# Performance work log

Measured on AMD Instinct MI355X. Metric: run time of the kernel, lower is better.

Reference implementation:

```python
import jax, jax.numpy as jnp
import numpy as np

EPS = 1e-3          # keras BatchNormalization default epsilon
DT = 0.2
LAM2 = 4.0          # lambda_diffusion**2 = 2.0**2
K = 5

def _bn(x, gamma, beta, mean, var):
    # inference-mode batch norm over channel (last) axis
    return (x - mean) * jax.lax.rsqrt(var + EPS) * gamma + beta

def _conv(x, w):
    # NHWC 'same' conv, stride 1, no bias
    return jax.lax.conv_general_dilated(x, w, (1, 1), 'SAME',
                                        dimension_numbers=('NHWC', 'HWIO', 'NHWC'))

def _sobel_edges(x):
    # tf.image.sobel_edges: per-channel 3x3 Sobel with REFLECT padding.
    # returns (dy, dx) matching sobel[...,0], sobel[...,1]
    p = jnp.pad(x, ((0, 0), (1, 1), (1, 1), (0, 0)), mode='reflect')
    dy = (p[:, 2:, :-2] + 2 * p[:, 2:, 1:-1] + p[:, 2:, 2:]) \
       - (p[:, :-2, :-2] + 2 * p[:, :-2, 1:-1] + p[:, :-2, 2:])
    dx = (p[:, :-2, 2:] + 2 * p[:, 1:-1, 2:] + p[:, 2:, 2:]) \
       - (p[:, :-2, :-2] + 2 * p[:, 1:-1, :-2] + p[:, 2:, :-2])
    return dy, dx

def setup_inputs() -> dict:
    key = jax.random.key(0)
    k1, k2, k3 = jax.random.split(key, 3)
    B, H, W, Cin, Cout = 16, 128, 128, 64, 64
    c = jnp.float32
    return {
        'x':   jax.random.normal(k1, (B, H, W, Cin), dtype=c),
        'f_w': jax.random.normal(k2, (3, 3, Cin, Cout), dtype=c) * 0.05,
        'g_w': jax.random.normal(k3, (3, 3, Cout, Cout), dtype=c) * 0.05,
        'bnf_gamma': jnp.ones((Cin,), c),  'bnf_beta': jnp.zeros((Cin,), c),
        'bnf_mean':  jnp.zeros((Cin,), c), 'bnf_var':  jnp.ones((Cin,), c),
        'bng_gamma': jnp.ones((Cout,), c), 'bng_beta': jnp.zeros((Cout,), c),
        'bng_mean':  jnp.zeros((Cout,), c),'bng_var':  jnp.ones((Cout,), c),
        'bno_gamma': jnp.ones((Cout,), c), 'bno_beta': jnp.zeros((Cout,), c),
        'bno_mean':  jnp.zeros((Cout,), c),'bno_var':  jnp.ones((Cout,), c),
    }

def reference(x, f_w, g_w,
              bnf_gamma, bnf_beta, bnf_mean, bnf_var,
              bng_gamma, bng_beta, bng_mean, bng_var,
              bno_gamma, bno_beta, bno_mean, bno_var):
    f = _conv(jax.nn.relu(_bn(x, bnf_gamma, bnf_beta, bnf_mean, bnf_var)), f_w)
    h = f
    g = _conv(jax.nn.relu(_bn(h, bng_gamma, bng_beta, bng_mean, bng_var)), g_w)
    g1 = g
    dy, dx = _sobel_edges(h)
    Dx = 1.0 / (dy * dy / LAM2 + 1.0)   # source: sobel[..., 0]
    Dy = 1.0 / (dx * dx / LAM2 + 1.0)   # source: sobel[..., 1]
    # NOTE: faithful to source — rolls on axis=2 (W) and axis=3 (channels in NHWC)
    ux = 0.5 * (jnp.roll(g, 1, axis=2) - jnp.roll(g, -1, axis=2))
    vy = 0.5 * (jnp.roll(g1, 1, axis=3) - jnp.roll(g1, -1, axis=3))
    Ax = g * DT
    Ay = g1 * DT
    Bx = Dx * DT
    By = Dy * DT
    E = (ux + vy) * DT
    D = 1.0 / (1.0 + 2 * Bx + 2 * By)
    h0 = h
    for _ in range(K):
        prev = h
        h = D * ((1 - 2 * Bx - 2 * By) * h0
                 - 2 * E * h
                 + (-Ax + 2 * Bx) * jnp.roll(h, 1, axis=2)
                 + ( Ax + 2 * Bx) * jnp.roll(h, -1, axis=2)
                 + (-Ay + 2 * By) * jnp.roll(h, 1, axis=3)
                 + ( Ay + 2 * By) * jnp.roll(h, -1, axis=3)
                 + 2 * DT * f)
        h0 = prev
    h = jax.nn.relu(_bn(h, bno_gamma, bno_beta, bno_mean, bno_var))
    return (h, g)
```

## Files before the change

### kernel.cpp

```cpp
#include <hip/hip_runtime.h>

#define HH 128
#define WW 128
#define CC 64
#define ROW (WW*CC)
#define SLOTB 128
#define ROWB (130*SLOTB)
#define FSTR 68

typedef _Float16 half8 __attribute__((ext_vector_type(8)));
typedef _Float16 half4v __attribute__((ext_vector_type(4)));
typedef float floatx4 __attribute__((ext_vector_type(4)));

__device__ inline floatx4 rcp4(floatx4 v)
{
    floatx4 r;
    r[0] = __builtin_amdgcn_rcpf(v[0]);
    r[1] = __builtin_amdgcn_rcpf(v[1]);
    r[2] = __builtin_amdgcn_rcpf(v[2]);
    r[3] = __builtin_amdgcn_rcpf(v[3]);
    return r;
}

__global__ __launch_bounds__(256)
void repack_w(const float* __restrict__ wf, const float* __restrict__ wg,
              _Float16* __restrict__ W2f, _Float16* __restrict__ W2g)
{
    int idx = blockIdx.x * 256 + threadIdx.x;
    int sel = idx >= 36864;
    int id  = sel ? idx - 36864 : idx;
    const float* src = sel ? wg : wf;
    _Float16* dst = sel ? W2g : W2f;
    int t = id >> 12, c = (id >> 6) & 63, o = id & 63;
    int kc = c >> 5, q = (c >> 3) & 3, j = c & 7;
    int pos = ((((t*2 + kc)*4 + q)*64 + o) << 3) + j;
    dst[pos] = (_Float16)src[id];
}

template<int BNIN, int EPI>
__global__ __launch_bounds__(512, 2)
void conv_mfma(const void* __restrict__ srcv, const _Float16* __restrict__ W2,
               _Float16* __restrict__ outH, float* __restrict__ outF,
               _Float16* __restrict__ y2,
               const float* __restrict__ ig, const float* __restrict__ ib,
               const float* __restrict__ imu, const float* __restrict__ iva,
               const float* __restrict__ og, const float* __restrict__ ob,
               const float* __restrict__ om, const float* __restrict__ ov)
{
    __shared__ __align__(16) char smem[69632];
    const int t = threadIdx.x;
    const int blk = ((blockIdx.x & 7) << 7) | (blockIdx.x >> 3);
    const int b = blk >> 6, i0 = (blk & 63) * 2;

    const int c8 = (t & 7) << 3;
    float scv[8], biv[8];
    if (BNIN) {
        #pragma unroll
        for (int j = 0; j < 8; ++j) {
            float s = ig[c8+j] * rsqrtf(iva[c8+j] + 1e-3f);
            scv[j] = s; biv[j] = ib[c8+j] - imu[c8+j]*s;
        }
    }

    if (t < 256) {
        int rr = t >> 6, s = (t >> 5) & 1;
        *(float*)(smem + rr*ROWB + (s ? 129*SLOTB : 0) + ((t & 31) << 2)) = 0.f;
    }

    if (BNIN) {
        for (int r = 0; r < 4; ++r) {
            int iy = i0 - 1 + r;
            bool inb = (iy >= 0) && (iy < HH);
            #pragma unroll
            for (int k = 0; k < 2; ++k) {
                int idx = t + (k << 9);
                int px = idx >> 3;
                half8 v = {0,0,0,0,0,0,0,0};
                if (inb) {
                    const float* gp = (const float*)srcv
                        + ((size_t)(b*HH + iy))*ROW + px*CC + c8;
                    float4 u0 = *(const float4*)gp;
                    float4 u1 = *(const float4*)(gp + 4);
                    v[0] = (_Float16)fmaxf(0.f, u0.x*scv[0] + biv[0]);
                    v[1] = (_Float16)fmaxf(0.f, u0.y*scv[1] + biv[1]);
                    v[2] = (_Float16)fmaxf(0.f, u0.z*scv[2] + biv[2]);
                    v[3] = (_Float16)fmaxf(0.f, u0.w*scv[3] + biv[3]);
                    v[4] = (_Float16)fmaxf(0.f, u1.x*scv[4] + biv[4]);
                    v[5] = (_Float16)fmaxf(0.f, u1.y*scv[5] + biv[5]);
                    v[6] = (_Float16)fmaxf(0.f, u1.z*scv[6] + biv[6]);
                    v[7] = (_Float16)fmaxf(0.f, u1.w*scv[7] + biv[7]);
                }
                int key = ((px + 1) & 7) << 4;
                *(half8*)(smem + r*ROWB + (px + 1)*SLOTB
                          + ((((t & 7) << 4)) ^ key)) = v;
            }
        }
    } else {
        const _Float16* src = (const _Float16*)srcv;
        #pragma unroll
        for (int r = 0; r < 4; ++r) {
            int iy = i0 - 1 + r;
            char* lb = smem + r*ROWB + SLOTB;
            if (iy >= 0 && iy < HH) {
                const _Float16* gp = src + (size_t)(b*HH + iy)*ROW;
                #pragma unroll
                for (int k = 0; k < 2; ++k) {
                    int eo = ((k << 9) + t) << 3;
                    __builtin_amdgcn_global_load_lds(
                        (const __attribute__((address_space(1))) void*)(gp + eo),
                        (__attribute__((address_space(3))) void*)(lb + (eo << 1)),
                        16, 0, 0);
                }
            } else {
                half8 z = {0,0,0,0,0,0,0,0};
                #pragma unroll
                for (int k = 0; k < 2; ++k)
                    *(half8*)(lb + (((k << 9) + t) << 4)) = z;
            }
        }
    }
    __syncthreads();

    const int wv = t >> 6, lane = t & 63;
    const int lm = lane & 15, quad = lane >> 4;
    const int r  = wv >> 2;
    const int px0 = (wv & 3) * 32;
    floatx4 z4 = {0.f,0.f,0.f,0.f};
    floatx4 acc[2][4];
    #pragma unroll
    for (int ms = 0; ms < 2; ++ms)
        #pragma unroll
        for (int nt = 0; nt < 4; ++nt) acc[ms][nt] = z4;

    #pragma unroll
    for (int tap = 0; tap < 9; ++tap) {
        const int di = tap / 3, dj = tap % 3;
        const int slot = px0 + lm + dj;
        const int key  = (slot & 7) << 4;
        const char* abase = smem + (r + di)*ROWB + slot*SLOTB;
        #pragma unroll
        for (int kc = 0; kc < 2; ++kc) {
            const char* ab = abase + ((kc*64 + quad*16) ^ key);
            half8 a0 = *(const half8*)(ab);
            half8 a1 = *(const half8*)(ab + 16*SLOTB);
            const _Float16* wb = W2 + (((tap*2 + kc)*4 + quad) << 9) + (lm << 3);
            half8 b0 = *(const half8*)(wb);
            half8 b1 = *(const half8*)(wb + 128);
            half8 b2 = *(const half8*)(wb + 256);
            half8 b3 = *(const half8*)(wb + 384);
            acc[0][0] = __builtin_amdgcn_mfma_f32_16x16x32_f16(a0, b0, acc[0][0], 0,0,0);
            acc[1][0] = __builtin_amdgcn_mfma_f32_16x16x32_f16(a1, b0, acc[1][0], 0,0,0);
            acc[0][1] = __builtin_amdgcn_mfma_f32_16x16x32_f16(a0, b1, acc[0][1], 0,0,0);
            acc[1][1] = __builtin_amdgcn_mfma_f32_16x16x32_f16(a1, b1, acc[1][1], 0,0,0);
            acc[0][2] = __builtin_amdgcn_mfma_f32_16x16x32_f16(a0, b2, acc[0][2], 0,0,0);
            acc[1][2] = __builtin_amdgcn_mfma_f32_16x16x32_f16(a1, b2, acc[1][2], 0,0,0);
            acc[0][3] = __builtin_amdgcn_mfma_f32_16x16x32_f16(a0, b3, acc[0][3], 0,0,0);
            acc[1][3] = __builtin_amdgcn_mfma_f32_16x16x32_f16(a1, b3, acc[1][3], 0,0,0);
        }
    }

    __syncthreads();
    float* sF = (float*)smem;
    #pragma unroll
    for (int nt = 0; nt < 4; ++nt) {
        int c = nt*16 + lm;
        #pragma unroll
        for (int ms = 0; ms < 2; ++ms) {
            int pix = r*128 + px0 + ms*16 + quad*4;
            floatx4 v = acc[ms][nt];
            #pragma unroll
            for (int rv = 0; rv < 4; ++rv)
                sF[(pix + rv)*FSTR + c] = v[rv];
        }
    }
    __syncthreads();

    const size_t gbase = ((size_t)(b*HH + i0)) * ROW;
    if (EPI) {
        float s8[8], bb8[8];
        #pragma unroll
        for (int j = 0; j < 8; ++j) {
            float ss = og[c8+j] * rsqrtf(ov[c8+j] + 1e-3f);
            s8[j] = ss; bb8[j] = ob[c8+j] - om[c8+j]*ss;
        }
        #pragma unroll
        for (int jj = 0; jj < 4; ++jj) {
            int chunk = (jj << 9) + t;
            int px = chunk >> 3;
            const float* sp = sF + px*FSTR + c8;
            floatx4 u0 = *(const floatx4*)(sp);
            floatx4 u1 = *(const floatx4*)(sp + 4);
            half8 hv, yv;
            #pragma unroll
            for (int j = 0; j < 4; ++j) {
                hv[j]   = (_Float16)u0[j];
                hv[4+j] = (_Float16)u1[j];
                yv[j]   = (_Float16)fmaxf(0.f, u0[j]*s8[j]   + bb8[j]);
                yv[4+j] = (_Float16)fmaxf(0.f, u1[j]*s8[4+j] + bb8[4+j]);
            }
            size_t oe = gbase + (size_t)px*CC + c8;
            *(half8*)(outH + oe) = hv;
            int pxr = px & 127;
            int key8 = ((pxr + 1) & 7) << 3;
            *(half8*)(y2 + gbase + (size_t)px*CC + (c8 ^ key8)) = yv;
        }
    } else {
        #pragma unroll
        for (int jj = 0; jj < 4; ++jj) {
            int chunk = (jj << 9) + t;
            int px = chunk >> 3;
            const float* sp = sF + px*FSTR + c8;
            size_t oe = gbase + (size_t)px*CC + c8;
            *(floatx4*)(outF + oe)     = *(const floatx4*)(sp);
            *(floatx4*)(outF + oe + 4) = *(const floatx4*)(sp + 4);
        }
    }
}

__global__ __launch_bounds__(1024, 2)
void diffuse(const _Float16* __restrict__ f, const float* __restrict__ g,
             float* __restrict__ out,
             const float* __restrict__ bog, const float* __restrict__ bob,
             const float* __restrict__ bom, const float* __restrict__ bov)
{
    __shared__ float B0[ROW], B1[ROW];
    const int t = threadIdx.x;
    const int rowb = ((blockIdx.x & 7) << 8) | (blockIdx.x >> 3);
    const int b = rowb >> 7, i = rowb & 127;
    const int im = (i == 0)    ? 1    : i - 1;
    const int ip = (i == HH-1) ? HH-2 : i + 1;
    const _Float16* fb  = f + (size_t)b * (HH*ROW);
    const _Float16* frm = fb + (size_t)im * ROW;
    const _Float16* fr0 = fb + (size_t)i  * ROW;
    const _Float16* frp = fb + (size_t)ip * ROW;
    const float* grow = g + (size_t)rowb * ROW;

    const int lane = t & 63;
    const int srcm = (lane & 48) | ((lane - 1) & 15);
    const int srcp = (lane & 48) | ((lane + 1) & 15);
    const int w0 = t >> 4, c0 = (t & 15) << 2;
    const int qch[2] = { t*4, t*4 + 4096 };
    const int wch[2] = { w0, w0 + 64 };

    #pragma unroll
    for (int k = 0; k < 2; ++k) {
        half4v vm = *(const half4v*)(frm + qch[k]);
        half4v vp = *(const half4v*)(frp + qch[k]);
        floatx4 a = { (float)vm[0], (float)vm[1], (float)vm[2], (float)vm[3] };
        floatx4 p = { (float)vp[0], (float)vp[1], (float)vp[2], (float)vp[3] };
        *(floatx4*)(B0 + qch[k]) = a;
        *(floatx4*)(B1 + qch[k]) = p;
    }
    __syncthreads();

    floatx4 Bx4[2], dxp4[2];
    #pragma unroll
    for (int k = 0; k < 2; ++k) {
        int w = wch[k];
        int wm = (w == 0)    ? 1      : w - 1;
        int wp = (w == WW-1) ? WW - 2 : w + 1;
        floatx4 am = *(const floatx4*)(B0 + wm*CC + c0);
        floatx4 a0 = *(const floatx4*)(B0 + w *CC + c0);
        floatx4 ap = *(const floatx4*)(B0 + wp*CC + c0);
        floatx4 bm = *(const floatx4*)(B1 + wm*CC + c0);
        floatx4 b0 = *(const floatx4*)(B1 + w *CC + c0);
        floatx4 bp = *(const floatx4*)(B1 + wp*CC + c0);
        floatx4 dy = (bm + 2.f*b0 + bp) - (am + 2.f*a0 + ap);
        Bx4[k]  = 0.2f * rcp4(dy*dy*0.25f + 1.f);
        dxp4[k] = (ap - am) + (bp - bm);
    }
    __syncthreads();

    #pragma unroll
    for (int k = 0; k < 2; ++k) {
        half4v v0 = *(const half4v*)(fr0 + qch[k]);
        floatx4 fv = { (float)v0[0], (float)v0[1], (float)v0[2], (float)v0[3] };
        *(floatx4*)(B0 + qch[k]) = fv;
        *(floatx4*)(B1 + qch[k]) = *(const floatx4*)(grow + qch[k]);
    }
    __syncthreads();

    floatx4 cR4[2], cL4[2], cU4[2], cH0[2], cEE[2], cF[2], h4[2], h04[2];
    #pragma unroll
    for (int k = 0; k < 2; ++k) {
        int w = wch[k];
        int wm = (w == 0)    ? 1      : w - 1;
        int wp = (w == WW-1) ? WW - 2 : w + 1;
        int wl = (w + WW - 1) & (WW - 1);
        int wr = (w + 1) & (WW - 1);
        floatx4 fm = *(const floatx4*)(B0 + wm*CC + c0);
        floatx4 fv = *(const floatx4*)(B0 + w *CC + c0);
        floatx4 fp = *(const floatx4*)(B0 + wp*CC + c0);
        floatx4 dx = dxp4[k] + 2.f*(fp - fm);
        floatx4 By = 0.2f * rcp4(dx*dx*0.25f + 1.f);
        floatx4 Bx = Bx4[k];
        floatx4 gv = *(const floatx4*)(B1 + w *CC + c0);
        floatx4 gl = *(const floatx4*)(B1 + wl*CC + c0);
        floatx4 gr = *(const floatx4*)(B1 + wr*CC + c0);
        float gdm = __shfl(gv[3], srcm, 64);
        float gup = __shfl(gv[0], srcp, 64);
        floatx4 gd = { gdm, gv[0], gv[1], gv[2] };
        floatx4 gu = { gv[1], gv[2], gv[3], gup };
        floatx4 E  = ((gl - gr) + (gd - gu)) * 0.1f;
        floatx4 Dd = rcp4(1.f + 2.f*Bx + 2.f*By);
        floatx4 P  = 2.f * Bx * Dd;
        floatx4 R  = 2.f * By * Dd;
        floatx4 Q  = (gv * 0.2f) * Dd;
        cR4[k] = P + Q;
        cL4[k] = P - Q;
        cU4[k] = R + Q;
        cH0[k] = 2.f*Dd - 1.f;
        cEE[k] = -2.f * E * Dd;
        cF[k]  = 0.4f * Dd * fv;
        h4[k] = fv; h04[k] = fv;
    }
    __syncthreads();

    int oWl[2], oWr[2];
    #pragma unroll
    for (int k = 0; k < 2; ++k) {
        int w = wch[k];
        oWl[k] = ((w + WW - 1) & (WW - 1))*CC + c0;
        oWr[k] = ((w + 1) & (WW - 1))*CC + c0;
    }

    float* cur = B0;
    float* oth = B1;
    for (int it = 0; it < 5; ++it) {
        #pragma unroll
        for (int k = 0; k < 2; ++k) {
            floatx4 hl = *(const floatx4*)(cur + oWl[k]);
            floatx4 hr = *(const floatx4*)(cur + oWr[k]);
            floatx4 hv = h4[k];
            float hdm = __shfl(hv[3], srcm, 64);
            float hup = __shfl(hv[0], srcp, 64);
            floatx4 hd = { hdm, hv[0], hv[1], hv[2] };
            floatx4 hu = { hv[1], hv[2], hv[3], hup };
            floatx4 cD = (cU4[k] - cR4[k]) + cL4[k];
            floatx4 hn = cH0[k]*h04[k] + cEE[k]*hv
                       + cR4[k]*hr + cL4[k]*hl
                       + cU4[k]*hu + cD*hd + cF[k];
            if (it < 4)
                *(floatx4*)(oth + qch[k]) = hn;
            h04[k] = hv; h4[k] = hn;
        }
        if (it < 4) {
            __syncthreads();
            float* tmp = cur; cur = oth; oth = tmp;
        }
    }

    floatx4 gg = *(const floatx4*)(bog + c0);
    floatx4 vv = *(const floatx4*)(bov + c0);
    floatx4 bb = *(const floatx4*)(bob + c0);
    floatx4 mm = *(const floatx4*)(bom + c0);
    floatx4 s4, bi4;
    #pragma unroll
    for (int j = 0; j < 4; ++j) s4[j] = gg[j] * rsqrtf(vv[j] + 1e-3f);
    bi4 = bb - mm*s4;
    float* op = out + (size_t)rowb * ROW;
    #pragma unroll
    for (int k = 0; k < 2; ++k) {
        floatx4 rr = h4[k]*s4 + bi4;
        #pragma unroll
        for (int j = 0; j < 4; ++j) rr[j] = fmaxf(0.f, rr[j]);
        *(floatx4*)(op + qch[k]) = rr;
    }
}

extern "C" void kernel_launch(void* const* d_in, const int* in_sizes, int n_in,
                              void* d_out, int out_size, void* d_ws, size_t ws_size,
                              hipStream_t stream)
{
    const float* x    = (const float*)d_in[0];
    const float* f_w  = (const float*)d_in[1];
    const float* g_w  = (const float*)d_in[2];
    const float* bnf_g = (const float*)d_in[3];
    const float* bnf_b = (const float*)d_in[4];
    const float* bnf_m = (const float*)d_in[5];
    const float* bnf_v = (const float*)d_in[6];
    const float* bng_g = (const float*)d_in[7];
    const float* bng_b = (const float*)d_in[8];
    const float* bng_m = (const float*)d_in[9];
    const float* bng_v = (const float*)d_in[10];
    const float* bno_g = (const float*)d_in[11];
    const float* bno_b = (const float*)d_in[12];
    const float* bno_m = (const float*)d_in[13];
    const float* bno_v = (const float*)d_in[14];

    float* out = (float*)d_out;
    const size_t N = (size_t)16 * HH * WW * CC;
    _Float16* y2   = (_Float16*)d_ws;
    _Float16* fbuf = y2 + N;
    _Float16* W2f  = y2 + 2*N;
    _Float16* W2g  = W2f + 36864;

    repack_w<<<288, 256, 0, stream>>>(f_w, g_w, W2f, W2g);
    conv_mfma<1,1><<<1024, 512, 0, stream>>>(x, W2f, fbuf, nullptr, y2,
                                             bnf_g, bnf_b, bnf_m, bnf_v,
                                             bng_g, bng_b, bng_m, bng_v);
    conv_mfma<0,0><<<1024, 512, 0, stream>>>(y2, W2g, nullptr, out + N, nullptr,
                                             nullptr, nullptr, nullptr, nullptr,
                                             nullptr, nullptr, nullptr, nullptr);
    diffuse<<<2048, 1024, 0, stream>>>(fbuf, out + N, out, bno_g, bno_b, bno_m, bno_v);
}
```

Before: 323.7 us.

## Preload half of conv weights into registers and remap wave tiling to 64px x 32ch

Changes each wave's output tile from 32 pixels x 64 channels to 64 pixels x 32 channels, so a wave only needs half the weight fragments. All 18 per-wave weight fragments are loaded into registers before the barrier, overlapping those global loads with the LDS fill. The inner loop then only reads activations from LDS. This costs many more VGPRs (36 half8 values), which may lower occupancy or cause spills, and doubles the LDS activation reads per wave.

```diff
diff --git a/kernel.cpp b/kernel.cpp
--- a/kernel.cpp
+++ b/kernel.cpp
@@ -119,18 +119,27 @@
             }
         }
     }
-    __syncthreads();
 
     const int wv = t >> 6, lane = t & 63;
     const int lm = lane & 15, quad = lane >> 4;
-    const int r  = wv >> 2;
-    const int px0 = (wv & 3) * 32;
+    const int r   = wv >> 2;
+    const int px0 = ((wv >> 1) & 1) * 64;
+    const int ch  = wv & 1;
+    half8 wp[18][2];
+    #pragma unroll
+    for (int s = 0; s < 18; ++s) {
+        const _Float16* wb = W2 + ((s*4 + quad) << 9) + (ch << 8) + (lm << 3);
+        wp[s][0] = *(const half8*)(wb);
+        wp[s][1] = *(const half8*)(wb + 128);
+    }
+    __syncthreads();
+
     floatx4 z4 = {0.f,0.f,0.f,0.f};
-    floatx4 acc[2][4];
-    #pragma unroll
-    for (int ms = 0; ms < 2; ++ms)
-        #pragma unroll
-        for (int nt = 0; nt < 4; ++nt) acc[ms][nt] = z4;
+    floatx4 acc[4][2];
+    #pragma unroll
+    for (int ms = 0; ms < 4; ++ms)
+        #pragma unroll
+        for (int nt = 0; nt < 2; ++nt) acc[ms][nt] = z4;
 
     #pragma unroll
     for (int tap = 0; tap < 9; ++tap) {
@@ -140,32 +149,30 @@
         const char* abase = smem + (r + di)*ROWB + slot*SLOTB;
         #pragma unroll
         for (int kc = 0; kc < 2; ++kc) {
+            const int s = tap*2 + kc;
             const char* ab = abase + ((kc*64 + quad*16) ^ key);
             half8 a0 = *(const half8*)(ab);
             half8 a1 = *(const half8*)(ab + 16*SLOTB);
-            const _Float16* wb = W2 + (((tap*2 + kc)*4 + quad) << 9) + (lm << 3);
-            half8 b0 = *(const half8*)(wb);
-            half8 b1 = *(const half8*)(wb + 128);
-            half8 b2 = *(const half8*)(wb + 256);
-            half8 b3 = *(const half8*)(wb + 384);
-            acc[0][0] = __builtin_amdgcn_mfma_f32_16x16x32_f16(a0, b0, acc[0][0], 0,0,0);
-            acc[1][0] = __builtin_amdgcn_mfma_f32_16x16x32_f16(a1, b0, acc[1][0], 0,0,0);
-            acc[0][1] = __builtin_amdgcn_mfma_f32_16x16x32_f16(a0, b1, acc[0][1], 0,0,0);
-            acc[1][1] = __builtin_amdgcn_mfma_f32_16x16x32_f16(a1, b1, acc[1][1], 0,0,0);
-            acc[0][2] = __builtin_amdgcn_mfma_f32_16x16x32_f16(a0, b2, acc[0][2], 0,0,0);
-            acc[1][2] = __builtin_amdgcn_mfma_f32_16x16x32_f16(a1, b2, acc[1][2], 0,0,0);
-            acc[0][3] = __builtin_amdgcn_mfma_f32_16x16x32_f16(a0, b3, acc[0][3], 0,0,0);
-            acc[1][3] = __builtin_amdgcn_mfma_f32_16x16x32_f16(a1, b3, acc[1][3], 0,0,0);
+            half8 a2 = *(const half8*)(ab + 32*SLOTB);
+            half8 a3 = *(const half8*)(ab + 48*SLOTB);
+            acc[0][0] = __builtin_amdgcn_mfma_f32_16x16x32_f16(a0, wp[s][0], acc[0][0], 0,0,0);
+            acc[1][0] = __builtin_amdgcn_mfma_f32_16x16x32_f16(a1, wp[s][0], acc[1][0], 0,0,0);
+            acc[2][0] = __builtin_amdgcn_mfma_f32_16x16x32_f16(a2, wp[s][0], acc[2][0], 0,0,0);
+            acc[3][0] = __builtin_amdgcn_mfma_f32_16x16x32_f16(a3, wp[s][0], acc[3][0], 0,0,0);
+            acc[0][1] = __builtin_amdgcn_mfma_f32_16x16x32_f16(a0, wp[s][1], acc[0][1], 0,0,0);
+            acc[1][1] = __builtin_amdgcn_mfma_f32_16x16x32_f16(a1, wp[s][1], acc[1][1], 0,0,0);
+            acc[2][1] = __builtin_amdgcn_mfma_f32_16x16x32_f16(a2, wp[s][1], acc[2][1], 0,0,0);
+            acc[3][1] = __builtin_amdgcn_mfma_f32_16x16x32_f16(a3, wp[s][1], acc[3][1], 0,0,0);
         }
     }
 
     __syncthreads();
     float* sF = (float*)smem;
     #pragma unroll
-    for (int nt = 0; nt < 4; ++nt) {
-        int c = nt*16 + lm;
-        #pragma unroll
-        for (int ms = 0; ms < 2; ++ms) {
+    for (int nt = 0; nt < 2; ++nt) {
+        int c = ch*32 + nt*16 + lm;
+        #pragma unroll
+        for (int ms = 0; ms < 4; ++ms) {
             int pix = r*128 + px0 + ms*16 + quad*4;
             floatx4 v = acc[ms][nt];
             #pragma unroll
```

New measurement: 331.2 us. 1.02x slower.
